# Performance work log

Measured on AMD Instinct MI355X. Metric: run time of the kernel, lower is better.

Reference implementation:

```python
import jax, jax.numpy as jnp
import numpy as np

D_MODEL = 512
NUM_HEADS = 8


def setup_inputs() -> dict:
    key = jax.random.key(0)
    ks = jax.random.split(key, 6)
    B, S, D = 4, 2048, D_MODEL
    Q = jax.random.normal(ks[0], (B, S, D), dtype=jnp.float32)
    K = jax.random.normal(ks[1], (B, S, D), dtype=jnp.float32)
    V = jax.random.normal(ks[2], (B, S, D), dtype=jnp.float32)
    # boolean mask, True = masked out; random so no row is fully masked
    mask = jax.random.randint(ks[3], (B, S, S), 0, 2).astype(jnp.bool_)
    scale = 1.0 / np.sqrt(D)
    Wq = jax.random.normal(ks[4], (D, D), dtype=jnp.float32) * scale
    Wo = jax.random.normal(ks[5], (D, D), dtype=jnp.float32) * scale
    return {"Q": Q, "K": K, "V": V, "mask": mask, "Wq": Wq, "Wo": Wo}


def reference(Q, K, V, mask, Wq, Wo):
    B, S, D = Q.shape
    H = NUM_HEADS
    dk = D // H
    # Faithful to the source: Q_Linear's weight (Wq) is applied to Q, K AND V
    # (K_Linear / V_Linear are dead parameters in the original module).
    q = (Q @ Wq.T).reshape(B, S, H, dk)
    k = (K @ Wq.T).reshape(B, S, H, dk)
    v = (V @ Wq.T).reshape(B, S, H, dk)
    # scores: [B, H, Sq, Sk]
    scores = jnp.einsum("bqhd,bkhd->bhqk", q, k)
    scores = jnp.where(mask[:, None, :, :], -jnp.inf, scores)
    w = jax.nn.softmax(scores / jnp.sqrt(jnp.asarray(dk, scores.dtype)), axis=-1)
    c = jnp.einsum("bhqk,bkhd->bqhd", w, v).reshape(B, S, D)
    return c @ Wo.T
```

## Files before the change

### kernel.cpp

```cpp
#include <hip/hip_runtime.h>
#include <math.h>

#define B_ 4
#define S_ 2048
#define D_ 512
#define H_ 8
#define DK_ 64
#define MROWS (B_ * S_)

typedef short bf16x8 __attribute__((ext_vector_type(8)));
typedef float f32x4 __attribute__((ext_vector_type(4)));

static __device__ __forceinline__ unsigned short f2bf(float x) {
    unsigned int u = __float_as_uint(x);
    return (unsigned short)((u + 0x7FFFu + ((u >> 16) & 1u)) >> 16);
}
static __device__ __forceinline__ unsigned int cvt_pk_bf16(float a, float b) {
    unsigned int r;
    asm("v_cvt_pk_bf16_f32 %0, %1, %2" : "=v"(r) : "v"(a), "v"(b));
    return r;
}
static __device__ __forceinline__ float exp2_fast(float x) {
    float r;
    asm("v_exp_f32 %0, %1" : "=v"(r) : "v"(x));
    return r;
}
static __device__ __forceinline__ void gld_lds16(const unsigned short* g, unsigned short* l) {
    __builtin_amdgcn_global_load_lds(
        (const __attribute__((address_space(1))) unsigned int*)g,
        (__attribute__((address_space(3))) unsigned int*)l, 16, 0, 0);
}

#define NXE (MROWS * D_)
#define NWE (D_ * D_)
#define CAST_BLOCKS ((3 * NXE + 2 * NWE) / 8 / 256)
#define MASK_BLOCKS (B_ * S_ * S_ / 256)

__global__ __launch_bounds__(256) void prep(const float* __restrict__ Q,
                                            const float* __restrict__ K,
                                            const float* __restrict__ V,
                                            const float* __restrict__ Wq,
                                            const float* __restrict__ Wo,
                                            const void* __restrict__ mask,
                                            unsigned short* __restrict__ Qb,
                                            unsigned short* __restrict__ Kb,
                                            unsigned short* __restrict__ Vb,
                                            unsigned short* __restrict__ Wqb,
                                            unsigned short* __restrict__ Wob,
                                            unsigned long long* __restrict__ mb) {
    if (blockIdx.x < CAST_BLOCKS) {
        const int NA = NXE / 8;
        const int NWn = NWE / 8;
        int id = blockIdx.x * 256 + threadIdx.x;
        const float* src;
        unsigned short* dst;
        if (id < 3 * NA) {
            int a = id / NA, r = id - a * NA;
            src = (a == 0 ? Q : a == 1 ? K : V) + (size_t)r * 8;
            dst = (a == 0 ? Qb : a == 1 ? Kb : Vb) + (size_t)r * 8;
        } else {
            int r = id - 3 * NA;
            int a = r / NWn; r -= a * NWn;
            src = (a == 0 ? Wq : Wo) + (size_t)r * 8;
            dst = (a == 0 ? Wqb : Wob) + (size_t)r * 8;
        }
        float4 x = *(const float4*)src;
        float4 y = *(const float4*)(src + 4);
        unsigned short u[8] = {f2bf(x.x), f2bf(x.y), f2bf(x.z), f2bf(x.w),
                               f2bf(y.x), f2bf(y.y), f2bf(y.z), f2bf(y.w)};
        *(uint4*)dst = *(const uint4*)u;
    } else {
        const int id = (blockIdx.x - CAST_BLOCKS) * 256 + threadIdx.x;
        unsigned int accw = 0;
        if ((threadIdx.x & 63) == 0) {
            const unsigned int* mw0 = (const unsigned int*)mask;
            #pragma unroll
            for (int i = 0; i < 16; ++i) accw |= mw0[i];
        }
        accw = __shfl(accw, 0);
        const bool bytemode = (accw & 0xFFFFFF00u) != 0u;
        int val;
        if (bytemode) val = ((const unsigned char*)mask)[id];
        else          val = ((const int*)mask)[id];
        unsigned long long w = __ballot(val != 0);
        if ((threadIdx.x & 63) == 0) mb[id >> 6] = w;
    }
}

__global__ __launch_bounds__(256) void proj3(const unsigned short* __restrict__ Qb,
                                             const unsigned short* __restrict__ Kb,
                                             const unsigned short* __restrict__ Vb,
                                             const unsigned short* __restrict__ Wqb,
                                             unsigned short* __restrict__ qs,
                                             unsigned short* __restrict__ kbo,
                                             unsigned short* __restrict__ vt) {
    __shared__ unsigned short As[128 * 40];
    __shared__ unsigned short Bs[128 * 40];
    const int t = threadIdx.x;
    const int w = t >> 6, lane = t & 63, col = lane & 15, quad = lane >> 4;
    const int bm = blockIdx.x * 128, bn = blockIdx.y * 128;
    const int z = blockIdx.z;
    const unsigned short* X = (z == 0) ? Qb : (z == 1) ? Kb : Vb;
    const int wm = (w >> 1) * 64, wn = (w & 1) * 64;
    const int srow = t >> 1, shalf = t & 1;

    const unsigned short* xg = X + (size_t)(bm + srow) * D_ + shalf * 16;
    const unsigned short* wg = Wqb + (size_t)(bn + srow) * D_ + shalf * 16;
    unsigned short* asw = &As[srow * 40 + shalf * 16];
    unsigned short* bsw = &Bs[srow * 40 + shalf * 16];

    f32x4 acc[4][4];
    #pragma unroll
    for (int i = 0; i < 4; ++i)
        #pragma unroll
        for (int j = 0; j < 4; ++j) acc[i][j] = (f32x4){0.f, 0.f, 0.f, 0.f};

    #pragma unroll 1
    for (int k0 = 0; k0 < D_; k0 += 32) {
        __syncthreads();
        {
            uint4 a0 = *(const uint4*)(xg + k0);
            uint4 a1 = *(const uint4*)(xg + k0 + 8);
            uint4 b0 = *(const uint4*)(wg + k0);
            uint4 b1 = *(const uint4*)(wg + k0 + 8);
            *(uint4*)asw = a0; *(uint4*)(asw + 8) = a1;
            *(uint4*)bsw = b0; *(uint4*)(bsw + 8) = b1;
        }
        __syncthreads();

        bf16x8 af[4], bg[4];
        #pragma unroll
        for (int i = 0; i < 4; ++i)
            af[i] = *(const bf16x8*)&As[(wm + i * 16 + col) * 40 + quad * 8];
        #pragma unroll
        for (int j = 0; j < 4; ++j)
            bg[j] = *(const bf16x8*)&Bs[(wn + j * 16 + col) * 40 + quad * 8];
        #pragma unroll
        for (int i = 0; i < 4; ++i)
            #pragma unroll
            for (int j = 0; j < 4; ++j)
                acc[i][j] = __builtin_amdgcn_mfma_f32_16x16x32_bf16(
                    af[i], bg[j], acc[i][j], 0, 0, 0);
    }

    if (z == 2) {
        #pragma unroll
        for (int i = 0; i < 4; ++i) {
            const int R = bm + wm + i * 16 + quad * 4;
            const int bb = R >> 11, s0 = R & (S_ - 1);
            #pragma unroll
            for (int j = 0; j < 4; ++j) {
                const int C = bn + wn + j * 16 + col;
                const int hh = C >> 6, dd = C & (DK_ - 1);
                ushort4 u = make_ushort4(f2bf(acc[i][j][0]), f2bf(acc[i][j][1]),
                                         f2bf(acc[i][j][2]), f2bf(acc[i][j][3]));
                *(ushort4*)&vt[(((size_t)bb * H_ + hh) * DK_ + dd) * S_ + s0] = u;
            }
        }
    } else {
        unsigned short* O = (z == 0) ? qs : kbo;
        const float scl = (z == 0) ? 0.18033688f : 1.0f;
        #pragma unroll
        for (int i = 0; i < 4; ++i)
            #pragma unroll
            for (int j = 0; j < 4; ++j) {
                const int R = bm + wm + i * 16 + quad * 4;
                const int C = bn + wn + j * 16 + col;
                #pragma unroll
                for (int r = 0; r < 4; ++r)
                    O[(size_t)(R + r) * D_ + C] = f2bf(acc[i][j][r] * scl);
            }
    }
}

__global__ __launch_bounds__(256) void gemm_out(const unsigned short* __restrict__ Xb,
                                                const unsigned short* __restrict__ Wob,
                                                float* __restrict__ Out) {
    __shared__ unsigned short As[128 * 40];
    __shared__ unsigned short Bs[128 * 40];
    const int t = threadIdx.x;
    const int w = t >> 6, lane = t & 63, col = lane & 15, quad = lane >> 4;
    const int bm = blockIdx.x * 128, bn = blockIdx.y * 128;
    const int wm = (w >> 1) * 64, wn = (w & 1) * 64;
    const int srow = t >> 1, shalf = t & 1;

    const unsigned short* xg = Xb + (size_t)(bm + srow) * D_ + shalf * 16;
    const unsigned short* wg = Wob + (size_t)(bn + srow) * D_ + shalf * 16;
    unsigned short* asw = &As[srow * 40 + shalf * 16];
    unsigned short* bsw = &Bs[srow * 40 + shalf * 16];

    f32x4 acc[4][4];
    #pragma unroll
    for (int i = 0; i < 4; ++i)
        #pragma unroll
        for (int j = 0; j < 4; ++j) acc[i][j] = (f32x4){0.f, 0.f, 0.f, 0.f};

    #pragma unroll 1
    for (int k0 = 0; k0 < D_; k0 += 32) {
        __syncthreads();
        {
            uint4 a0 = *(const uint4*)(xg + k0);
            uint4 a1 = *(const uint4*)(xg + k0 + 8);
            uint4 b0 = *(const uint4*)(wg + k0);
            uint4 b1 = *(const uint4*)(wg + k0 + 8);
            *(uint4*)asw = a0; *(uint4*)(asw + 8) = a1;
            *(uint4*)bsw = b0; *(uint4*)(bsw + 8) = b1;
        }
        __syncthreads();

        bf16x8 af[4], bg[4];
        #pragma unroll
        for (int i = 0; i < 4; ++i)
            af[i] = *(const bf16x8*)&As[(wm + i * 16 + col) * 40 + quad * 8];
        #pragma unroll
        for (int j = 0; j < 4; ++j)
            bg[j] = *(const bf16x8*)&Bs[(wn + j * 16 + col) * 40 + quad * 8];
        #pragma unroll
        for (int i = 0; i < 4; ++i)
            #pragma unroll
            for (int j = 0; j < 4; ++j)
                acc[i][j] = __builtin_amdgcn_mfma_f32_16x16x32_bf16(
                    af[i], bg[j], acc[i][j], 0, 0, 0);
    }

    #pragma unroll
    for (int i = 0; i < 4; ++i)
        #pragma unroll
        for (int j = 0; j < 4; ++j) {
            const int R = bm + wm + i * 16 + quad * 4;
            const int C = bn + wn + j * 16 + col;
            #pragma unroll
            for (int r = 0; r < 4; ++r)
                Out[(size_t)(R + r) * D_ + C] = acc[i][j][r];
        }
}

__global__ __launch_bounds__(256, 3) void attn_mfma(
        const unsigned short* __restrict__ qb,
        const unsigned short* __restrict__ kb,
        const unsigned short* __restrict__ vt,
        const unsigned long long* __restrict__ mb,
        unsigned short* __restrict__ o0,
        unsigned short* __restrict__ o1,
        float* __restrict__ l0,
        float* __restrict__ l1) {
    __shared__ unsigned short sm[25600];
    const int t = threadIdx.x;
    const int w = t >> 6;
    const int lane = t & 63;
    const int col = lane & 15;
    const int quad = lane >> 4;
    const int h = blockIdx.y;
    const int b = blockIdx.z >> 1;
    const int khalf = blockIdx.z & 1;
    const int bh = b * H_ + h;
    const int qrow0 = blockIdx.x * 128 + w * 32;

    unsigned short* opart = khalf ? o1 : o0;
    float* lpart = khalf ? l1 : l0;

    const int PS = 16384 + w * 2304;

    const unsigned int chk = cvt_pk_bf16(1.0f, 2.0f);
    const int dlo = ((chk & 0xFFFFu) == 0x3F80u) ? 0 : 16;
    const int dhi = 16 - dlo;

    bf16x8 aQ0[2], aQ1[2];
    #pragma unroll
    for (int s = 0; s < 2; ++s) {
        const unsigned short* qp =
            qb + (size_t)(b * S_ + qrow0 + s * 16 + col) * D_ + h * DK_ + quad * 8;
        aQ0[s] = *(const bf16x8*)(qp);
        aQ1[s] = *(const bf16x8*)(qp + 32);
    }

    bf16x8 ones;
    #pragma unroll
    for (int i = 0; i < 8; ++i) ones[i] = (short)0x3F80;

    f32x4 O[2][4];
    #pragma unroll
    for (int s = 0; s < 2; ++s)
        #pragma unroll
        for (int g = 0; g < 4; ++g) O[s][g] = (f32x4){0.f, 0.f, 0.f, 0.f};
    f32x4 lacc[2];
    lacc[0] = (f32x4){0.f, 0.f, 0.f, 0.f};
    lacc[1] = (f32x4){0.f, 0.f, 0.f, 0.f};

    const float CREF = 8.656170245f;
    const int kbeg = khalf * (S_ / 2);

    const int ln8 = lane >> 3;
    const int fs8 = ((lane & 7) ^ ln8) * 8;
    const int r0 = w * 16 + ln8;
    const unsigned short* pK0 = kb + (size_t)(b * S_ + kbeg + r0) * D_ + h * DK_ + fs8;
    const unsigned short* pK1 = pK0 + 8 * D_;
    const unsigned short* pV0 = vt + ((size_t)bh * DK_ + r0) * S_ + kbeg + fs8;
    const unsigned short* pV1 = pV0 + 8 * S_;

    const unsigned long long* mbase =
        mb + (size_t)(b * S_ + qrow0 + quad * 4) * (S_ / 64) + (kbeg >> 6);

    gld_lds16(pK0, &sm[w * 1024]);
    gld_lds16(pK1, &sm[w * 1024 + 512]);
    gld_lds16(pV0, &sm[4096 + w * 1024]);
    gld_lds16(pV1, &sm[4096 + w * 1024 + 512]);
    pK0 += 64 * D_; pK1 += 64 * D_; pV0 += 64; pV1 += 64;

    unsigned long long mc[8];
    #pragma unroll
    for (int s = 0; s < 2; ++s)
        #pragma unroll
        for (int r = 0; r < 4; ++r)
            mc[s * 4 + r] = mbase[(s * 16 + r) * 32];

    const int ps0 = (quad ^ (col & 7)) * 8;
    const int ps1 = ps0 ^ 32;

    #pragma unroll 1
    for (int ti = 0; ti < 16; ++ti) {
        unsigned long long mn[8];
        if (ti < 15) {
            const int nb = (ti & 1) ? 0 : 8192;
            gld_lds16(pK0, &sm[nb + w * 1024]);
            gld_lds16(pK1, &sm[nb + w * 1024 + 512]);
            gld_lds16(pV0, &sm[nb + 4096 + w * 1024]);
            gld_lds16(pV1, &sm[nb + 4096 + w * 1024 + 512]);
            pK0 += 64 * D_; pK1 += 64 * D_; pV0 += 64; pV1 += 64;
            #pragma unroll
            for (int s = 0; s < 2; ++s)
                #pragma unroll
                for (int r = 0; r < 4; ++r)
                    mn[s * 4 + r] = mbase[(s * 16 + r) * 32 + ti + 1];
            __asm__ __volatile__("s_waitcnt vmcnt(12)" ::: "memory");
        } else {
            __asm__ __volatile__("s_waitcnt vmcnt(0)" ::: "memory");
        }
        __builtin_amdgcn_s_barrier();

        const int KB = (ti & 1) ? 8192 : 0;
        const int VB = KB + 4096;

        f32x4 sc[2][4];
        __builtin_amdgcn_s_setprio(1);
        #pragma unroll
        for (int g = 0; g < 4; ++g) {
            const int krow = KB + (g * 16 + col) * 64;
            bf16x8 bk0 = *(const bf16x8*)&sm[krow + ps0];
            bf16x8 bk1 = *(const bf16x8*)&sm[krow + ps1];
            #pragma unroll
            for (int s = 0; s < 2; ++s) {
                f32x4 z = {0.f, 0.f, 0.f, 0.f};
                z = __builtin_amdgcn_mfma_f32_16x16x32_bf16(aQ0[s], bk0, z, 0, 0, 0);
                z = __builtin_amdgcn_mfma_f32_16x16x32_bf16(aQ1[s], bk1, z, 0, 0, 0);
                sc[s][g] = z;
            }
        }
        __builtin_amdgcn_s_setprio(0);

        #pragma unroll
        for (int s = 0; s < 2; ++s) {
            #pragma unroll
            for (int r = 0; r < 4; ++r) {
                const unsigned long long sh = mc[s * 4 + r] >> col;
                const unsigned int lo = (unsigned int)sh;
                const unsigned int hi = (unsigned int)(sh >> 32);
                float p0 = exp2_fast(((lo & 1u)       ? -1e30f : sc[s][0][r]) - CREF);
                float p1 = exp2_fast(((lo & 0x10000u) ? -1e30f : sc[s][1][r]) - CREF);
                float p2 = exp2_fast(((hi & 1u)       ? -1e30f : sc[s][2][r]) - CREF);
                float p3 = exp2_fast(((hi & 0x10000u) ? -1e30f : sc[s][3][r]) - CREF);
                const unsigned int u01 = cvt_pk_bf16(p0, p1);
                const unsigned int u23 = cvt_pk_bf16(p2, p3);
                const int prow = PS + (s * 16 + quad * 4 + r) * 72 + col;
                sm[prow + dlo]      = (unsigned short)u01;
                sm[prow + dhi]      = (unsigned short)(u01 >> 16);
                sm[prow + 32 + dlo] = (unsigned short)u23;
                sm[prow + 32 + dhi] = (unsigned short)(u23 >> 16);
            }
        }
        __asm__ __volatile__("s_waitcnt lgkmcnt(0)" ::: "memory");

        bf16x8 aP0[2], aP1[2];
        #pragma unroll
        for (int s = 0; s < 2; ++s) {
            aP0[s] = *(const bf16x8*)&sm[PS + (s * 16 + col) * 72 + quad * 8];
            aP1[s] = *(const bf16x8*)&sm[PS + (s * 16 + col) * 72 + 32 + quad * 8];
        }

        __builtin_amdgcn_s_setprio(1);
        #pragma unroll
        for (int s = 0; s < 2; ++s) {
            lacc[s] = __builtin_amdgcn_mfma_f32_16x16x32_bf16(aP0[s], ones, lacc[s], 0, 0, 0);
            lacc[s] = __builtin_amdgcn_mfma_f32_16x16x32_bf16(aP1[s], ones, lacc[s], 0, 0, 0);
        }

        #pragma unroll
        for (int g = 0; g < 4; ++g) {
            const int vrow = VB + (g * 16 + col) * 64;
            bf16x8 bv0 = *(const bf16x8*)&sm[vrow + ps0];
            bf16x8 bv1 = *(const bf16x8*)&sm[vrow + ps1];
            #pragma unroll
            for (int s = 0; s < 2; ++s) {
                O[s][g] = __builtin_amdgcn_mfma_f32_16x16x32_bf16(aP0[s], bv0, O[s][g], 0, 0, 0);
                O[s][g] = __builtin_amdgcn_mfma_f32_16x16x32_bf16(aP1[s], bv1, O[s][g], 0, 0, 0);
            }
        }
        __builtin_amdgcn_s_setprio(0);

        if (ti < 15) {
            #pragma unroll
            for (int i = 0; i < 8; ++i) mc[i] = mn[i];
            __builtin_amdgcn_s_barrier();
        }
    }

    #pragma unroll
    for (int s = 0; s < 2; ++s)
        #pragma unroll
        for (int r = 0; r < 4; ++r) {
            const int row = b * S_ + qrow0 + s * 16 + quad * 4 + r;
            #pragma unroll
            for (int g = 0; g < 4; ++g)
                opart[(size_t)row * D_ + h * DK_ + g * 16 + col] = f2bf(O[s][g][r]);
            if (col == 0) lpart[(size_t)row * H_ + h] = lacc[s][r];
        }
}

__global__ __launch_bounds__(256) void combine(const unsigned short* __restrict__ o0,
                                               const unsigned short* __restrict__ o1,
                                               const float* __restrict__ l0,
                                               const float* __restrict__ l1,
                                               unsigned short* __restrict__ cb) {
    const int id = blockIdx.x * 256 + threadIdx.x;
    const size_t base = (size_t)id * 8;
    const int row = (int)(base >> 9);
    const int hh = ((int)base & (D_ - 1)) >> 6;
    uint4 ua = *(const uint4*)(o0 + base);
    uint4 ub = *(const uint4*)(o1 + base);
    const float inv = 1.0f / (l0[(size_t)row * H_ + hh] + l1[(size_t)row * H_ + hh]);
    const unsigned short* pa = (const unsigned short*)&ua;
    const unsigned short* pb = (const unsigned short*)&ub;
    unsigned short out[8];
    #pragma unroll
    for (int i = 0; i < 8; ++i) {
        float fa = __uint_as_float((unsigned int)pa[i] << 16);
        float fb = __uint_as_float((unsigned int)pb[i] << 16);
        out[i] = f2bf((fa + fb) * inv);
    }
    *(uint4*)(cb + base) = *(const uint4*)out;
}

extern "C" void kernel_launch(void* const* d_in, const int* in_sizes, int n_in,
                              void* d_out, int out_size, void* d_ws, size_t ws_size,
                              hipStream_t stream) {
    const float* Q    = (const float*)d_in[0];
    const float* K    = (const float*)d_in[1];
    const float* V    = (const float*)d_in[2];
    const void*  mask = d_in[3];
    const float* Wq   = (const float*)d_in[4];
    const float* Wo   = (const float*)d_in[5];
    float* out = (float*)d_out;

    const size_t NX = (size_t)MROWS * D_;
    const size_t NW = (size_t)D_ * D_;
    unsigned short* Qb   = (unsigned short*)d_ws;
    unsigned short* Kb   = Qb + NX;
    unsigned short* Vb   = Kb + NX;
    unsigned short* Wqb  = Vb + NX;
    unsigned short* Wob  = Wqb + NW;
    unsigned short* qbuf = Wob + NW;
    unsigned short* kbuf = qbuf + NX;
    unsigned short* vtb  = kbuf + NX;
    unsigned short* cbuf = vtb + NX;
    unsigned long long* mb = (unsigned long long*)(cbuf + NX);

    unsigned short* o0 = Qb;
    unsigned short* o1 = Kb;
    float* l0 = (float*)Vb;
    float* l1 = l0 + (size_t)MROWS * H_;

    prep<<<dim3(CAST_BLOCKS + MASK_BLOCKS), dim3(256), 0, stream>>>(
        Q, K, V, Wq, Wo, mask, Qb, Kb, Vb, Wqb, Wob, mb);

    proj3<<<dim3(MROWS / 128, D_ / 128, 3), dim3(256), 0, stream>>>(
        Qb, Kb, Vb, Wqb, qbuf, kbuf, vtb);

    attn_mfma<<<dim3(S_ / 128, H_, B_ * 2), dim3(256), 0, stream>>>(
        qbuf, kbuf, vtb, mb, o0, o1, l0, l1);

    combine<<<dim3((int)(NX / 8 / 256)), dim3(256), 0, stream>>>(o0, o1, l0, l1, cbuf);

    gemm_out<<<dim3(MROWS / 128, D_ / 128), dim3(256), 0, stream>>>(cbuf, Wob, out);
}
```

Before: 288.7 us.

## Keep P in registers via transposed QK^T and 16x16x16 MFMA for PV

```diff
diff --git a/kernel.cpp b/kernel.cpp
--- a/kernel.cpp
+++ b/kernel.cpp
@@ -9,6 +9,7 @@
 #define MROWS (B_ * S_)
 
 typedef short bf16x8 __attribute__((ext_vector_type(8)));
+typedef short bf16x4 __attribute__((ext_vector_type(4)));
 typedef float f32x4 __attribute__((ext_vector_type(4)));
 
 static __device__ __forceinline__ unsigned short f2bf(float x) {
@@ -29,6 +30,18 @@
     __builtin_amdgcn_global_load_lds(
         (const __attribute__((address_space(1))) unsigned int*)g,
         (__attribute__((address_space(3))) unsigned int*)l, 16, 0, 0);
+}
+static __device__ __forceinline__ f32x4 mfma16(bf16x4 a, bf16x4 b, f32x4 c) {
+#if __has_builtin(__builtin_amdgcn_mfma_f32_16x16x16_bf16)
+    return __builtin_amdgcn_mfma_f32_16x16x16_bf16(a, b, c, 0, 0, 0);
+#elif __has_builtin(__builtin_amdgcn_mfma_f32_16x16x16bf16_1k)
+    return __builtin_amdgcn_mfma_f32_16x16x16bf16_1k(a, b, c, 0, 0, 0);
+#else
+    f32x4 d;
+    asm volatile("v_mfma_f32_16x16x16_bf16 %0, %1, %2, %0"
+                 : "=v"(d) : "v"(a), "v"(b), "0"(c));
+    return d;
+#endif
 }
 
 #define NXE (MROWS * D_)
@@ -235,7 +248,7 @@
         }
 }
 
-__global__ __launch_bounds__(256, 3) void attn_mfma(
+__global__ __launch_bounds__(256, 4) void attn_mfma(
         const unsigned short* __restrict__ qb,
         const unsigned short* __restrict__ kb,
         const unsigned short* __restrict__ vt,
@@ -244,7 +257,7 @@
         unsigned short* __restrict__ o1,
         float* __restrict__ l0,
         float* __restrict__ l1) {
-    __shared__ unsigned short sm[25600];
+    __shared__ unsigned short sm[16384];
     const int t = threadIdx.x;
     const int w = t >> 6;
     const int lane = t & 63;
@@ -259,11 +272,8 @@
     unsigned short* opart = khalf ? o1 : o0;
     float* lpart = khalf ? l1 : l0;
 
-    const int PS = 16384 + w * 2304;
-
     const unsigned int chk = cvt_pk_bf16(1.0f, 2.0f);
-    const int dlo = ((chk & 0xFFFFu) == 0x3F80u) ? 0 : 16;
-    const int dhi = 16 - dlo;
+    const bool ablow = ((chk & 0xFFFFu) == 0x3F80u);
 
     bf16x8 aQ0[2], aQ1[2];
     #pragma unroll
@@ -274,9 +284,9 @@
         aQ1[s] = *(const bf16x8*)(qp + 32);
     }
 
-    bf16x8 ones;
-    #pragma unroll
-    for (int i = 0; i < 8; ++i) ones[i] = (short)0x3F80;
+    bf16x4 ones4;
+    #pragma unroll
+    for (int i = 0; i < 4; ++i) ones4[i] = (short)0x3F80;
 
     f32x4 O[2][4];
     #pragma unroll
@@ -298,8 +308,9 @@
     const unsigned short* pV0 = vt + ((size_t)bh * DK_ + r0) * S_ + kbeg + fs8;
     const unsigned short* pV1 = pV0 + 8 * S_;
 
-    const unsigned long long* mbase =
-        mb + (size_t)(b * S_ + qrow0 + quad * 4) * (S_ / 64) + (kbeg >> 6);
+    const unsigned long long* mbase0 =
+        mb + (size_t)(b * S_ + qrow0 + col) * (S_ / 64) + (kbeg >> 6);
+    const unsigned long long* mbase1 = mbase0 + 16 * (S_ / 64);
 
     gld_lds16(pK0, &sm[w * 1024]);
     gld_lds16(pK1, &sm[w * 1024 + 512]);
@@ -307,19 +318,17 @@
     gld_lds16(pV1, &sm[4096 + w * 1024 + 512]);
     pK0 += 64 * D_; pK1 += 64 * D_; pV0 += 64; pV1 += 64;
 
-    unsigned long long mc[8];
-    #pragma unroll
-    for (int s = 0; s < 2; ++s)
-        #pragma unroll
-        for (int r = 0; r < 4; ++r)
-            mc[s * 4 + r] = mbase[(s * 16 + r) * 32];
-
-    const int ps0 = (quad ^ (col & 7)) * 8;
+    const int c7 = col & 7;
+    const int ps0 = (quad ^ c7) * 8;
     const int ps1 = ps0 ^ 32;
+    const int vq = quad >> 1;
+    const int vr = (quad & 1) * 4;
 
     #pragma unroll 1
     for (int ti = 0; ti < 16; ++ti) {
-        unsigned long long mn[8];
+        unsigned long long mw0 = mbase0[ti];
+        unsigned long long mw1 = mbase1[ti];
+        __builtin_amdgcn_sched_barrier(0);
         if (ti < 15) {
             const int nb = (ti & 1) ? 0 : 8192;
             gld_lds16(pK0, &sm[nb + w * 1024]);
@@ -327,14 +336,9 @@
             gld_lds16(pV0, &sm[nb + 4096 + w * 1024]);
             gld_lds16(pV1, &sm[nb + 4096 + w * 1024 + 512]);
             pK0 += 64 * D_; pK1 += 64 * D_; pV0 += 64; pV1 += 64;
-            #pragma unroll
-            for (int s = 0; s < 2; ++s)
-                #pragma unroll
-                for (int r = 0; r < 4; ++r)
-                    mn[s * 4 + r] = mbase[(s * 16 + r) * 32 + ti + 1];
-            __asm__ __volatile__("s_waitcnt vmcnt(12)" ::: "memory");
+            __asm__ __volatile__("s_waitcnt vmcnt(6)" ::: "memory");
         } else {
-            __asm__ __volatile__("s_waitcnt vmcnt(0)" ::: "memory");
+            __asm__ __volatile__("s_waitcnt vmcnt(2)" ::: "memory");
         }
         __builtin_amdgcn_s_barrier();
 
@@ -351,67 +355,56 @@
             #pragma unroll
             for (int s = 0; s < 2; ++s) {
                 f32x4 z = {0.f, 0.f, 0.f, 0.f};
-                z = __builtin_amdgcn_mfma_f32_16x16x32_bf16(aQ0[s], bk0, z, 0, 0, 0);
-                z = __builtin_amdgcn_mfma_f32_16x16x32_bf16(aQ1[s], bk1, z, 0, 0, 0);
+                z = __builtin_amdgcn_mfma_f32_16x16x32_bf16(bk0, aQ0[s], z, 0, 0, 0);
+                z = __builtin_amdgcn_mfma_f32_16x16x32_bf16(bk1, aQ1[s], z, 0, 0, 0);
                 sc[s][g] = z;
             }
         }
         __builtin_amdgcn_s_setprio(0);
 
+        bf16x4 pf[2][4];
         #pragma unroll
         for (int s = 0; s < 2; ++s) {
-            #pragma unroll
-            for (int r = 0; r < 4; ++r) {
-                const unsigned long long sh = mc[s * 4 + r] >> col;
-                const unsigned int lo = (unsigned int)sh;
-                const unsigned int hi = (unsigned int)(sh >> 32);
-                float p0 = exp2_fast(((lo & 1u)       ? -1e30f : sc[s][0][r]) - CREF);
-                float p1 = exp2_fast(((lo & 0x10000u) ? -1e30f : sc[s][1][r]) - CREF);
-                float p2 = exp2_fast(((hi & 1u)       ? -1e30f : sc[s][2][r]) - CREF);
-                float p3 = exp2_fast(((hi & 0x10000u) ? -1e30f : sc[s][3][r]) - CREF);
-                const unsigned int u01 = cvt_pk_bf16(p0, p1);
-                const unsigned int u23 = cvt_pk_bf16(p2, p3);
-                const int prow = PS + (s * 16 + quad * 4 + r) * 72 + col;
-                sm[prow + dlo]      = (unsigned short)u01;
-                sm[prow + dhi]      = (unsigned short)(u01 >> 16);
-                sm[prow + 32 + dlo] = (unsigned short)u23;
-                sm[prow + 32 + dhi] = (unsigned short)(u23 >> 16);
+            const unsigned long long mws = s ? mw1 : mw0;
+            #pragma unroll
+            for (int g = 0; g < 4; ++g) {
+                const unsigned int m4 =
+                    (unsigned int)(mws >> (g * 16 + quad * 4)) & 0xFu;
+                float p0 = exp2_fast(((m4 & 1u) ? -1e30f : sc[s][g][0]) - CREF);
+                float p1 = exp2_fast(((m4 & 2u) ? -1e30f : sc[s][g][1]) - CREF);
+                float p2 = exp2_fast(((m4 & 4u) ? -1e30f : sc[s][g][2]) - CREF);
+                float p3 = exp2_fast(((m4 & 8u) ? -1e30f : sc[s][g][3]) - CREF);
+                const unsigned int w0 = ablow ? cvt_pk_bf16(p0, p1)
+                                              : cvt_pk_bf16(p1, p0);
+                const unsigned int w1 = ablow ? cvt_pk_bf16(p2, p3)
+                                              : cvt_pk_bf16(p3, p2);
+                union { unsigned long long u; bf16x4 v; } cv;
+                cv.u = (unsigned long long)w0 | ((unsigned long long)w1 << 32);
+                pf[s][g] = cv.v;
             }
         }
-        __asm__ __volatile__("s_waitcnt lgkmcnt(0)" ::: "memory");
-
-        bf16x8 aP0[2], aP1[2];
-        #pragma unroll
-        for (int s = 0; s < 2; ++s) {
-            aP0[s] = *(const bf16x8*)&sm[PS + (s * 16 + col) * 72 + quad * 8];
-            aP1[s] = *(const bf16x8*)&sm[PS + (s * 16 + col) * 72 + 32 + quad * 8];
-        }
 
         __builtin_amdgcn_s_setprio(1);
         #pragma unroll
-        for (int s = 0; s < 2; ++s) {
-            lacc[s] = __builtin_amdgcn_mfma_f32_16x16x32_bf16(aP0[s], ones, lacc[s], 0, 0, 0);
-            lacc[s] = __builtin_amdgcn_mfma_f32_16x16x32_bf16(aP1[s], ones, lacc[s], 0, 0, 0);
-        }
+        for (int s = 0; s < 2; ++s)
+            #pragma unroll
+            for (int g = 0; g < 4; ++g)
+                lacc[s] = mfma16(pf[s][g], ones4, lacc[s]);
 
         #pragma unroll
         for (int g = 0; g < 4; ++g) {
-            const int vrow = VB + (g * 16 + col) * 64;
-            bf16x8 bv0 = *(const bf16x8*)&sm[vrow + ps0];
-            bf16x8 bv1 = *(const bf16x8*)&sm[vrow + ps1];
-            #pragma unroll
-            for (int s = 0; s < 2; ++s) {
-                O[s][g] = __builtin_amdgcn_mfma_f32_16x16x32_bf16(aP0[s], bv0, O[s][g], 0, 0, 0);
-                O[s][g] = __builtin_amdgcn_mfma_f32_16x16x32_bf16(aP1[s], bv1, O[s][g], 0, 0, 0);
+            const int vx = VB + ((2 * g + vq) ^ c7) * 8 + vr;
+            #pragma unroll
+            for (int db = 0; db < 4; ++db) {
+                bf16x4 vf = *(const bf16x4*)&sm[vx + (db * 16 + col) * 64];
+                #pragma unroll
+                for (int s = 0; s < 2; ++s)
+                    O[s][db] = mfma16(pf[s][g], vf, O[s][db]);
             }
         }
         __builtin_amdgcn_s_setprio(0);
 
-        if (ti < 15) {
-            #pragma unroll
-            for (int i = 0; i < 8; ++i) mc[i] = mn[i];
-            __builtin_amdgcn_s_barrier();
-        }
+        __builtin_amdgcn_s_barrier();
     }
 
     #pragma unroll
```

New measurement: 277.1 us. -4.0%, faster.
